# Optimization experiments

Measured on AMD Instinct MI355X. Metric: run time of the kernel, lower is better.

Reference implementation:

```python
import jax, jax.numpy as jnp
import numpy as np

DA = 256      # aux input feature dim
DENSE = 512   # SLAM dense units


def setup_inputs() -> dict:
    key = jax.random.key(0)
    k1, k2, k3, k4 = jax.random.split(key, 4)
    x_main = jax.random.normal(k1, (1, 128, 512, 256), dtype=jnp.float32)  # [1,T,M,K]
    x_aux = jax.random.normal(k2, (256, 128, DA), dtype=jnp.float32)       # [K,T,Da]
    W = jax.random.normal(k3, (DA, DENSE), dtype=jnp.float32) / np.sqrt(DA)
    b = jax.random.normal(k4, (DENSE,), dtype=jnp.float32) * 0.01
    return {"x_main": x_main, "x_aux": x_aux, "W": W, "b": b}


def reference(x_main, x_aux, W, b):
    # SLAM aux dense (+relu), applied to every aux slice at once: [K,T,Da] -> [K,T,dense]
    aux_out = jax.nn.relu(jnp.einsum("ktd,de->kte", x_aux, W) + b)
    main = jnp.squeeze(x_main, axis=0)  # [T,M,K]
    # per-slice matmul main[t] @ aux_out[:,t,:] batched over T
    stacked = jnp.einsum("tmk,kte->tme", main, aux_out)  # [T,M,dense]
    # expand_dims(-1) then expand_dims(0)
    return stacked[None, :, :, :, None]  # [1,T,M,dense,1]
```

## Files before the change

### kernel.cpp

```cpp
#include <hip/hip_runtime.h>


typedef __attribute__((ext_vector_type(8))) short  bf16x8;
typedef __attribute__((ext_vector_type(4))) float  f32x4;
typedef __attribute__((ext_vector_type(4))) unsigned int uint4v;
typedef __attribute__((ext_vector_type(2))) unsigned int uint2v;

#define T_DIM 128
#define M_DIM 512
#define K_DIM 256
#define DA    256
#define DENSE 512
#define CHUNK_T_STRIDE 131072
#define CHUNK_G_STRIDE 4096

__device__ __forceinline__ unsigned short f2bf(float f) {
    unsigned u = __builtin_bit_cast(unsigned, f);
    unsigned r = (u + 0x7fffu + ((u >> 16) & 1u)) >> 16;
    return (unsigned short)r;
}
__device__ __forceinline__ unsigned pack2(float lo, float hi) {
    return (unsigned)f2bf(lo) | ((unsigned)f2bf(hi) << 16);
}

__global__ __launch_bounds__(256) void wchunk_kernel(const float* __restrict__ W,
                                                     unsigned short* __restrict__ Wc) {
    int c = blockIdx.x * 256 + threadIdx.x;
    int g = c >> 9;
    int e = c & 511;
    float f[8];
#pragma unroll
    for (int j = 0; j < 8; ++j) f[j] = W[(g * 8 + j) * DENSE + e];
    uint4v w;
    w.x = pack2(f[0], f[1]); w.y = pack2(f[2], f[3]);
    w.z = pack2(f[4], f[5]); w.w = pack2(f[6], f[7]);
    *reinterpret_cast<uint4v*>(Wc + (size_t)c * 8) = w;
}

__global__ __launch_bounds__(256) void xmchunk_kernel(const float* __restrict__ xmain,
                                                      unsigned short* __restrict__ xmc) {
    __shared__ unsigned short lds[64 * 256];
    const int mb = blockIdx.x * 64;
    const int t  = blockIdx.y;
    const int tid = threadIdx.x, lane = tid & 63, wid = tid >> 6;
    char* ldsb = reinterpret_cast<char*>(lds);
#pragma unroll
    for (int j = 0; j < 16; ++j) {
        int mr = wid + 4 * j;
        const float* src = xmain + ((size_t)(t * M_DIM + mb + mr)) * K_DIM + lane * 4;
        f32x4 v = *reinterpret_cast<const f32x4*>(src);
        uint2v o; o.x = pack2(v.x, v.y); o.y = pack2(v.z, v.w);
        int bofs = mr * 512 + ((lane * 8) ^ ((mr & 7) << 4));
        *reinterpret_cast<uint2v*>(ldsb + bofs) = o;
    }
    __syncthreads();
#pragma unroll
    for (int i = 0; i < 8; ++i) {
        int g = wid * 8 + i;
        int bofs = lane * 512 + ((g * 16) ^ ((lane & 7) << 4));
        uint4v c = *reinterpret_cast<const uint4v*>(ldsb + bofs);
        *reinterpret_cast<uint4v*>(xmc + (size_t)t * CHUNK_T_STRIDE + (size_t)g * CHUNK_G_STRIDE
                                   + (size_t)(mb + lane) * 8) = c;
    }
}

__global__ __launch_bounds__(256) void aux_kernel(const float* __restrict__ xaux,
                                                  const unsigned short* __restrict__ Wc,
                                                  const float* __restrict__ bias,
                                                  unsigned short* __restrict__ auxc) {
    __shared__ unsigned short xa[64 * 264];
    const int bid = blockIdx.x;
    const int swz = (bid & 7) * 128 + (bid >> 3);
    const int t  = swz >> 3;
    const int r  = swz & 7;
    const int kb = (r >> 1) * 64;
    const int eb = (r & 1) * 256;
    const int tid = threadIdx.x, lane = tid & 63, wid = tid >> 6;
    const int l15 = lane & 15, lg = lane >> 4;
    char* xab = reinterpret_cast<char*>(xa);

#pragma unroll
    for (int j = 0; j < 16; ++j) {
        int kr = wid + 4 * j;
        const float* src = xaux + ((size_t)(kb + kr) * T_DIM + t) * DA + lane * 4;
        f32x4 v = *reinterpret_cast<const f32x4*>(src);
        uint2v o; o.x = pack2(v.x, v.y); o.y = pack2(v.z, v.w);
        *reinterpret_cast<uint2v*>(xab + kr * 528 + lane * 8) = o;
    }
    __syncthreads();

    const int we = wid * 64;
    f32x4 acc[4][4];
#pragma unroll
    for (int i = 0; i < 4; ++i)
#pragma unroll
        for (int j = 0; j < 4; ++j) acc[i][j] = (f32x4)0.0f;

#define AUX_LOAD_WF(dst, dsv)                                                              \
    do {                                                                                   \
        _Pragma("unroll") for (int j = 0; j < 4; ++j) {                                    \
            int e = eb + we + j * 16 + l15;                                                \
            dst[j] = *reinterpret_cast<const bf16x8*>(                                     \
                Wc + (size_t)((dsv) * 4 + lg) * CHUNK_G_STRIDE + (size_t)e * 8);           \
        }                                                                                  \
    } while (0)

#define AUX_COMPUTE(wfc, dsv)                                                              \
    do {                                                                                   \
        bf16x8 xf[4];                                                                      \
        _Pragma("unroll") for (int i = 0; i < 4; ++i)                                      \
            xf[i] = *reinterpret_cast<const bf16x8*>(                                      \
                xab + (i * 16 + l15) * 528 + ((dsv) * 4 + lg) * 16);                       \
        _Pragma("unroll") for (int i = 0; i < 4; ++i)                                      \
            _Pragma("unroll") for (int j = 0; j < 4; ++j)                                  \
                acc[i][j] = __builtin_amdgcn_mfma_f32_16x16x32_bf16(xf[i], wfc[j], acc[i][j], 0, 0, 0); \
    } while (0)

    bf16x8 wfA[4], wfB[4];
    AUX_LOAD_WF(wfA, 0);
#pragma unroll
    for (int ds = 0; ds < 8; ds += 2) {
        AUX_LOAD_WF(wfB, ds + 1);
        AUX_COMPUTE(wfA, ds);
        if (ds + 2 < 8) { AUX_LOAD_WF(wfA, ds + 2); }
        AUX_COMPUTE(wfB, ds + 1);
    }
#undef AUX_LOAD_WF
#undef AUX_COMPUTE

#pragma unroll
    for (int i = 0; i < 4; ++i) {
        int k0 = kb + i * 16 + lg * 4;
#pragma unroll
        for (int j = 0; j < 4; ++j) {
            int e = eb + we + j * 16 + l15;
            float bv = bias[e];
            float v0 = fmaxf(acc[i][j].x + bv, 0.0f);
            float v1 = fmaxf(acc[i][j].y + bv, 0.0f);
            float v2 = fmaxf(acc[i][j].z + bv, 0.0f);
            float v3 = fmaxf(acc[i][j].w + bv, 0.0f);
            uint2 o; o.x = pack2(v0, v1); o.y = pack2(v2, v3);
            size_t idx = (size_t)t * CHUNK_T_STRIDE + (size_t)(k0 >> 3) * CHUNK_G_STRIDE
                       + (size_t)e * 8 + (k0 & 7);
            *reinterpret_cast<uint2*>(auxc + idx) = o;
        }
    }
}

__global__ __launch_bounds__(256) void main_kernel(const unsigned short* __restrict__ xmc,
                                                   const unsigned short* __restrict__ auxc,
                                                   float* __restrict__ out) {
    const int bid = blockIdx.x;
    const int swz = ((bid & 7) << 8) | (bid >> 3);
    const int t   = swz >> 4;
    const int r4  = swz & 15;
    const int eb  = (r4 & 3) * 128;
    const int mb  = (r4 >> 2) * 128;
    const int lane = threadIdx.x & 63, wid = threadIdx.x >> 6;
    const int wm = (wid & 1) * 64;
    const int we = (wid >> 1) * 64;
    const int l15 = lane & 15, lg = lane >> 4;

    const unsigned short* At = auxc + (size_t)t * CHUNK_T_STRIDE;
    const unsigned short* Bt = xmc  + (size_t)t * CHUNK_T_STRIDE;

    f32x4 acc[4][4];
#pragma unroll
    for (int i = 0; i < 4; ++i)
#pragma unroll
        for (int j = 0; j < 4; ++j) acc[i][j] = (f32x4)0.0f;

#define MAIN_LOAD(afd, mfd, ksv)                                                           \
    do {                                                                                   \
        _Pragma("unroll") for (int i = 0; i < 4; ++i)                                      \
            afd[i] = *reinterpret_cast<const bf16x8*>(                                     \
                At + (size_t)((ksv) * 4 + lg) * CHUNK_G_STRIDE                             \
                   + (size_t)(eb + we + i * 16 + l15) * 8);                                \
        _Pragma("unroll") for (int j = 0; j < 4; ++j)                                      \
            mfd[j] = *reinterpret_cast<const bf16x8*>(                                     \
                Bt + (size_t)((ksv) * 4 + lg) * CHUNK_G_STRIDE                             \
                   + (size_t)(mb + wm + j * 16 + l15) * 8);                                \
    } while (0)

#define MAIN_COMPUTE(afd, mfd)                                                             \
    do {                                                                                   \
        _Pragma("unroll") for (int i = 0; i < 4; ++i)                                      \
            _Pragma("unroll") for (int j = 0; j < 4; ++j)                                  \
                acc[i][j] = __builtin_amdgcn_mfma_f32_16x16x32_bf16(afd[i], mfd[j], acc[i][j], 0, 0, 0); \
    } while (0)

    bf16x8 afA[4], afB[4], mfA[4], mfB[4];
    MAIN_LOAD(afA, mfA, 0);
#pragma unroll
    for (int ks = 0; ks < 8; ks += 2) {
        MAIN_LOAD(afB, mfB, ks + 1);
        MAIN_COMPUTE(afA, mfA);
        if (ks + 2 < 8) { MAIN_LOAD(afA, mfA, ks + 2); }
        MAIN_COMPUTE(afB, mfB);
    }
#undef MAIN_LOAD
#undef MAIN_COMPUTE

#pragma unroll
    for (int i = 0; i < 4; ++i) {
        int e0 = eb + we + i * 16 + lg * 4;
#pragma unroll
        for (int j = 0; j < 4; ++j) {
            int m = mb + wm + j * 16 + l15;
            *reinterpret_cast<f32x4*>(out + (size_t)t * M_DIM * DENSE + (size_t)m * DENSE + e0) = acc[i][j];
        }
    }
}

extern "C" void kernel_launch(void* const* d_in, const int* in_sizes, int n_in,
                              void* d_out, int out_size, void* d_ws, size_t ws_size,
                              hipStream_t stream) {
    const float* x_main = (const float*)d_in[0];
    const float* x_aux  = (const float*)d_in[1];
    const float* W      = (const float*)d_in[2];
    const float* b      = (const float*)d_in[3];
    float* out = (float*)d_out;

    unsigned short* Wc   = (unsigned short*)d_ws;
    unsigned short* auxc = (unsigned short*)((char*)d_ws + (1u << 19));
    unsigned short* xmc  = (unsigned short*)((char*)d_ws + (1u << 19) + (1u << 25));

    wchunk_kernel<<<64, 256, 0, stream>>>(W, Wc);
    xmchunk_kernel<<<dim3(8, 128), 256, 0, stream>>>(x_main, xmc);
    aux_kernel<<<1024, 256, 0, stream>>>(x_aux, Wc, b, auxc);
    main_kernel<<<2048, 256, 0, stream>>>(xmc, auxc, out);
}
```

Measured before the change: 257.1 us.

## Fuse x_main bf16 conversion into main GEMM via double-buffered LDS staging

Removes the separate xmchunk pre-pass that converted x_main to a chunked bf16 layout in workspace. The main kernel now reads fp32 x_main directly, converts to bf16 in registers, and stages tiles through double-buffered padded LDS with a barrier per k-step. This saves one full write and re-read of the converted x_main and one kernel launch. In exchange, each x_main tile is re-read in fp32 by the four blocks covering different e ranges, and the main loop gains LDS traffic and synchronisation.

```diff
diff --git a/kernel.cpp b/kernel.cpp
--- a/kernel.cpp
+++ b/kernel.cpp
@@ -35,33 +35,6 @@
     w.x = pack2(f[0], f[1]); w.y = pack2(f[2], f[3]);
     w.z = pack2(f[4], f[5]); w.w = pack2(f[6], f[7]);
     *reinterpret_cast<uint4v*>(Wc + (size_t)c * 8) = w;
-}
-
-__global__ __launch_bounds__(256) void xmchunk_kernel(const float* __restrict__ xmain,
-                                                      unsigned short* __restrict__ xmc) {
-    __shared__ unsigned short lds[64 * 256];
-    const int mb = blockIdx.x * 64;
-    const int t  = blockIdx.y;
-    const int tid = threadIdx.x, lane = tid & 63, wid = tid >> 6;
-    char* ldsb = reinterpret_cast<char*>(lds);
-#pragma unroll
-    for (int j = 0; j < 16; ++j) {
-        int mr = wid + 4 * j;
-        const float* src = xmain + ((size_t)(t * M_DIM + mb + mr)) * K_DIM + lane * 4;
-        f32x4 v = *reinterpret_cast<const f32x4*>(src);
-        uint2v o; o.x = pack2(v.x, v.y); o.y = pack2(v.z, v.w);
-        int bofs = mr * 512 + ((lane * 8) ^ ((mr & 7) << 4));
-        *reinterpret_cast<uint2v*>(ldsb + bofs) = o;
-    }
-    __syncthreads();
-#pragma unroll
-    for (int i = 0; i < 8; ++i) {
-        int g = wid * 8 + i;
-        int bofs = lane * 512 + ((g * 16) ^ ((lane & 7) << 4));
-        uint4v c = *reinterpret_cast<const uint4v*>(ldsb + bofs);
-        *reinterpret_cast<uint4v*>(xmc + (size_t)t * CHUNK_T_STRIDE + (size_t)g * CHUNK_G_STRIDE
-                                   + (size_t)(mb + lane) * 8) = c;
-    }
 }
 
 __global__ __launch_bounds__(256) void aux_kernel(const float* __restrict__ xaux,
@@ -147,22 +120,29 @@
     }
 }
 
-__global__ __launch_bounds__(256) void main_kernel(const unsigned short* __restrict__ xmc,
+#define MS_STRIDE 72
+#define MS_BUF    (128 * MS_STRIDE)
+__global__ __launch_bounds__(256) void main_kernel(const float* __restrict__ xmain,
                                                    const unsigned short* __restrict__ auxc,
                                                    float* __restrict__ out) {
+    __shared__ char ms[2 * MS_BUF];
     const int bid = blockIdx.x;
     const int swz = ((bid & 7) << 8) | (bid >> 3);
     const int t   = swz >> 4;
     const int r4  = swz & 15;
     const int eb  = (r4 & 3) * 128;
     const int mb  = (r4 >> 2) * 128;
-    const int lane = threadIdx.x & 63, wid = threadIdx.x >> 6;
+    const int tid  = threadIdx.x;
+    const int lane = tid & 63, wid = tid >> 6;
     const int wm = (wid & 1) * 64;
     const int we = (wid >> 1) * 64;
     const int l15 = lane & 15, lg = lane >> 4;
 
-    const unsigned short* At = auxc + (size_t)t * CHUNK_T_STRIDE;
-    const unsigned short* Bt = xmc  + (size_t)t * CHUNK_T_STRIDE;
+    const float* At = xmain + (size_t)t * M_DIM * K_DIM;
+    const unsigned short* Ct = auxc + (size_t)t * CHUNK_T_STRIDE;
+
+    const int srow = tid >> 3;
+    const int skof = tid & 7;
 
     f32x4 acc[4][4];
 #pragma unroll
@@ -170,36 +150,57 @@
 #pragma unroll
         for (int j = 0; j < 4; ++j) acc[i][j] = (f32x4)0.0f;
 
-#define MAIN_LOAD(afd, mfd, ksv)                                                           \
-    do {                                                                                   \
-        _Pragma("unroll") for (int i = 0; i < 4; ++i)                                      \
-            afd[i] = *reinterpret_cast<const bf16x8*>(                                     \
-                At + (size_t)((ksv) * 4 + lg) * CHUNK_G_STRIDE                             \
-                   + (size_t)(eb + we + i * 16 + l15) * 8);                                \
-        _Pragma("unroll") for (int j = 0; j < 4; ++j)                                      \
-            mfd[j] = *reinterpret_cast<const bf16x8*>(                                     \
-                Bt + (size_t)((ksv) * 4 + lg) * CHUNK_G_STRIDE                             \
-                   + (size_t)(mb + wm + j * 16 + l15) * 8);                                \
-    } while (0)
-
-#define MAIN_COMPUTE(afd, mfd)                                                             \
-    do {                                                                                   \
-        _Pragma("unroll") for (int i = 0; i < 4; ++i)                                      \
-            _Pragma("unroll") for (int j = 0; j < 4; ++j)                                  \
-                acc[i][j] = __builtin_amdgcn_mfma_f32_16x16x32_bf16(afd[i], mfd[j], acc[i][j], 0, 0, 0); \
-    } while (0)
-
-    bf16x8 afA[4], afB[4], mfA[4], mfB[4];
-    MAIN_LOAD(afA, mfA, 0);
-#pragma unroll
-    for (int ks = 0; ks < 8; ks += 2) {
-        MAIN_LOAD(afB, mfB, ks + 1);
-        MAIN_COMPUTE(afA, mfA);
-        if (ks + 2 < 8) { MAIN_LOAD(afA, mfA, ks + 2); }
-        MAIN_COMPUTE(afB, mfB);
-    }
-#undef MAIN_LOAD
-#undef MAIN_COMPUTE
+#define MS_LOAD(regs, ksv)                                                                 \
+    do {                                                                                   \
+        _Pragma("unroll") for (int p = 0; p < 4; ++p)                                      \
+            regs[p] = *reinterpret_cast<const f32x4*>(                                     \
+                At + (size_t)(mb + p * 32 + srow) * K_DIM + (ksv) * 32 + skof * 4);        \
+    } while (0)
+
+#define MS_WRITE(regs, bufv)                                                               \
+    do {                                                                                   \
+        _Pragma("unroll") for (int p = 0; p < 4; ++p) {                                    \
+            uint2v o;                                                                      \
+            o.x = pack2(regs[p].x, regs[p].y);                                             \
+            o.y = pack2(regs[p].z, regs[p].w);                                             \
+            *reinterpret_cast<uint2v*>(ms + (bufv) * MS_BUF                                \
+                                          + (p * 32 + srow) * MS_STRIDE + skof * 8) = o;   \
+        }                                                                                  \
+    } while (0)
+
+    f32x4 sreg[4];
+    MS_LOAD(sreg, 0);
+    MS_WRITE(sreg, 0);
+    __syncthreads();
+
+#pragma unroll
+    for (int ks = 0; ks < 8; ++ks) {
+        const int cur = ks & 1;
+        if (ks < 7) MS_LOAD(sreg, ks + 1);
+
+        bf16x8 af[4], mf[4];
+#pragma unroll
+        for (int i = 0; i < 4; ++i)
+            af[i] = *reinterpret_cast<const bf16x8*>(
+                Ct + (size_t)(ks * 4 + lg) * CHUNK_G_STRIDE
+                   + (size_t)(eb + we + i * 16 + l15) * 8);
+#pragma unroll
+        for (int j = 0; j < 4; ++j)
+            mf[j] = *reinterpret_cast<const bf16x8*>(
+                ms + cur * MS_BUF + (wm + j * 16 + l15) * MS_STRIDE + lg * 16);
+#pragma unroll
+        for (int i = 0; i < 4; ++i)
+#pragma unroll
+            for (int j = 0; j < 4; ++j)
+                acc[i][j] = __builtin_amdgcn_mfma_f32_16x16x32_bf16(af[i], mf[j], acc[i][j], 0, 0, 0);
+
+        if (ks < 7) {
+            MS_WRITE(sreg, cur ^ 1);
+            __syncthreads();
+        }
+    }
+#undef MS_LOAD
+#undef MS_WRITE
 
 #pragma unroll
     for (int i = 0; i < 4; ++i) {
@@ -223,10 +224,8 @@
 
     unsigned short* Wc   = (unsigned short*)d_ws;
     unsigned short* auxc = (unsigned short*)((char*)d_ws + (1u << 19));
-    unsigned short* xmc  = (unsigned short*)((char*)d_ws + (1u << 19) + (1u << 25));
 
     wchunk_kernel<<<64, 256, 0, stream>>>(W, Wc);
-    xmchunk_kernel<<<dim3(8, 128), 256, 0, stream>>>(x_main, xmc);
     aux_kernel<<<1024, 256, 0, stream>>>(x_aux, Wc, b, auxc);
-    main_kernel<<<2048, 256, 0, stream>>>(xmc, auxc, out);
-}
+    main_kernel<<<2048, 256, 0, stream>>>(x_main, auxc, out);
+}
```

Result: slower. 269.3 us (+4.7%).
